# Kernel optimization log

Measured on AMD Instinct MI355X. Metric: run time of the kernel, lower is better.

Reference implementation:

```python
import jax, jax.numpy as jnp
import numpy as np

H = 1024      # hidden_size
V = 50257     # output_size (vocab)
L = 64        # max_length


def setup_inputs() -> dict:
    key = jax.random.key(0)
    ks = jax.random.split(key, 14)
    s = 1.0 / np.sqrt(H)
    return {
        "input": jax.random.randint(ks[0], (1,), 0, V, dtype=jnp.int64),
        "hidden": jax.random.normal(ks[1], (1, 1, H), dtype=jnp.float32),
        "encoder_outputs": jax.random.normal(ks[2], (L, H), dtype=jnp.float32),
        "emb": jax.random.normal(ks[3], (V, H), dtype=jnp.float32),
        "attn_W": jax.random.normal(ks[4], (L, 2 * H), dtype=jnp.float32) * s,
        "attn_b": jax.random.normal(ks[5], (L,), dtype=jnp.float32) * s,
        "comb_W": jax.random.normal(ks[6], (H, 2 * H), dtype=jnp.float32) * s,
        "comb_b": jax.random.normal(ks[7], (H,), dtype=jnp.float32) * s,
        "w_ih": jax.random.normal(ks[8], (3 * H, H), dtype=jnp.float32) * s,
        "w_hh": jax.random.normal(ks[9], (3 * H, H), dtype=jnp.float32) * s,
        "b_ih": jax.random.normal(ks[10], (3 * H,), dtype=jnp.float32) * s,
        "b_hh": jax.random.normal(ks[11], (3 * H,), dtype=jnp.float32) * s,
        "out_W": jax.random.normal(ks[12], (V, H), dtype=jnp.float32) * s,
        "out_b": jax.random.normal(ks[13], (V,), dtype=jnp.float32) * s,
    }


def reference(input, hidden, encoder_outputs, emb, attn_W, attn_b,
              comb_W, comb_b, w_ih, w_hh, b_ih, b_hh, out_W, out_b):
    # embedded: [1, H]  (dropout is identity, p effectively 0 at inference)
    embedded = emb[input[0]][None, :]
    h0 = hidden[0]  # [1, H]

    # additive-style attention over encoder_outputs [L, H]
    attn_logits = jnp.concatenate([embedded, h0], axis=1) @ attn_W.T + attn_b  # [1, L]
    attn_weights = jax.nn.softmax(attn_logits, axis=1)                          # [1, L]
    attn_applied = attn_weights @ encoder_outputs                               # [1, H]

    x = jnp.concatenate([embedded, attn_applied], axis=1) @ comb_W.T + comb_b  # [1, H]
    x = jax.nn.relu(x)

    # single-step GRU cell (PyTorch gate ordering: r, z, n)
    gi = x @ w_ih.T + b_ih    # [1, 3H]
    gh = h0 @ w_hh.T + b_hh   # [1, 3H]
    i_r, i_z, i_n = jnp.split(gi, 3, axis=1)
    h_r, h_z, h_n = jnp.split(gh, 3, axis=1)
    r = jax.nn.sigmoid(i_r + h_r)
    z = jax.nn.sigmoid(i_z + h_z)
    n = jnp.tanh(i_n + r * h_n)
    h_new = (1.0 - z) * n + z * h0  # [1, H]

    out = jax.nn.log_softmax(h_new @ out_W.T + out_b, axis=1)  # [1, V]
    return out, h_new[None, :, :], attn_weights
```

## Files before the change

kernel.cpp:

```cpp
#include <hip/hip_runtime.h>
#include <math.h>

constexpr int H = 1024;
constexpr int V = 50257;
constexpr int L = 64;

constexpr int NBLKD = 512;

constexpr int OFF_ALOG = 0;
constexpr int OFF_GH   = 64;
constexpr int OFF_X    = 64 + 3 * H;
constexpr int OFF_LOG  = OFF_X + H;
constexpr int OFF_PAIR = OFF_LOG + V;

__device__ __forceinline__ float wsum(float v) {
#pragma unroll
    for (int off = 32; off > 0; off >>= 1) v += __shfl_xor(v, off);
    return v;
}
__device__ __forceinline__ float wmax(float v) {
#pragma unroll
    for (int off = 32; off > 0; off >>= 1) v = fmaxf(v, __shfl_xor(v, off));
    return v;
}

__device__ __forceinline__ float dot4(float4 a, float4 b) {
    return a.x * b.x + a.y * b.y + a.z * b.z + a.w * b.w;
}

__device__ __forceinline__ float dotN(const float* __restrict__ w,
                                      const float* __restrict__ v,
                                      int lane, int n4) {
    const float4* w4 = reinterpret_cast<const float4*>(w);
    const float4* v4 = reinterpret_cast<const float4*>(v);
    float acc = 0.f;
    for (int it = 0; it < n4; ++it)
        acc += dot4(w4[lane + it * 64], v4[lane + it * 64]);
    return acc;
}

__device__ __forceinline__ void dot1024x2(const float* __restrict__ wa,
                                          const float* __restrict__ wb,
                                          const float* __restrict__ v,
                                          int lane, float& oa, float& ob) {
    const float4* a4 = reinterpret_cast<const float4*>(wa);
    const float4* b4 = reinterpret_cast<const float4*>(wb);
    const float4* v4 = reinterpret_cast<const float4*>(v);
    float sa = 0.f, sb = 0.f;
#pragma unroll
    for (int it = 0; it < 4; ++it) {
        const float4 x = a4[lane + it * 64];
        const float4 y = b4[lane + it * 64];
        const float4 u = v4[lane + it * 64];
        sa += dot4(x, u);
        sb += dot4(y, u);
    }
    oa = sa; ob = sb;
}

__device__ __forceinline__ void msmerge(float& m, float& s, float m2, float s2) {
    const float M = fmaxf(m, m2);
    s = s * expf(m - M) + s2 * expf(m2 - M);
    m = M;
}

__global__ __launch_bounds__(256) void kA(const long long* __restrict__ idx_p,
                                          const float* __restrict__ hid,
                                          const float* __restrict__ emb,
                                          const float* __restrict__ attn_W,
                                          const float* __restrict__ attn_b,
                                          const float* __restrict__ w_hh,
                                          const float* __restrict__ b_hh,
                                          float* __restrict__ ws) {
    const int tid = threadIdx.x;
    const int lane = tid & 63, wid = tid >> 6;
    if (blockIdx.x < 64) {
        const int l = blockIdx.x;
        const int idx = (int)idx_p[0];
        const float4* w4 = reinterpret_cast<const float4*>(attn_W + (size_t)l * (2 * H));
        const float4* e4 = reinterpret_cast<const float4*>(emb + (size_t)idx * H);
        const float4* h4 = reinterpret_cast<const float4*>(hid);
        float acc = dot4(w4[tid], e4[tid]) + dot4(w4[tid + 256], h4[tid]);
        acc = wsum(acc);
        __shared__ float sred[4];
        if (lane == 0) sred[wid] = acc;
        __syncthreads();
        if (tid == 0)
            ws[OFF_ALOG + l] = sred[0] + sred[1] + sred[2] + sred[3] + attn_b[l];
    } else {
        __shared__ __align__(16) float4 sv[256];
        sv[tid] = reinterpret_cast<const float4*>(hid)[tid];
        __syncthreads();
        const int row = (blockIdx.x - 64) * 4 + wid;
        float acc = wsum(dotN(w_hh + (size_t)row * H,
                              reinterpret_cast<const float*>(sv), lane, 4));
        if (lane == 0) ws[OFF_GH + row] = acc + b_hh[row];
    }
}

__global__ __launch_bounds__(256) void kB(const long long* __restrict__ idx_p,
                                          const float* __restrict__ emb,
                                          const float* __restrict__ enc,
                                          const float* __restrict__ comb_W,
                                          const float* __restrict__ comb_b,
                                          float* __restrict__ ws,
                                          float* __restrict__ out) {
    __shared__ float wls[L];
    __shared__ __align__(16) float4 sx[512];
    const int tid = threadIdx.x;
    if (tid < L) {
        const float lg = ws[OFF_ALOG + tid];
        const float m = wmax(lg);
        const float e = expf(lg - m);
        const float s = wsum(e);
        wls[tid] = e / s;
        if (blockIdx.x == 0) out[V + H + tid] = e / s;
    }
    __syncthreads();
    const int idx = (int)idx_p[0];
    sx[tid] = reinterpret_cast<const float4*>(emb + (size_t)idx * H)[tid];
    {
        const float4* e4 = reinterpret_cast<const float4*>(enc);
        float4 a4 = {0.f, 0.f, 0.f, 0.f};
#pragma unroll 8
        for (int l = 0; l < L; ++l) {
            const float wl = wls[l];
            const float4 v = e4[l * 256 + tid];
            a4.x += wl * v.x; a4.y += wl * v.y;
            a4.z += wl * v.z; a4.w += wl * v.w;
        }
        sx[256 + tid] = a4;
    }
    __syncthreads();
    const int lane = tid & 63, wid = tid >> 6;
    const int row = blockIdx.x * 4 + wid;
    float acc = wsum(dotN(comb_W + (size_t)row * (2 * H),
                          reinterpret_cast<const float*>(sx), lane, 8));
    if (lane == 0) ws[OFF_X + row] = fmaxf(acc + comb_b[row], 0.f);
}

__global__ __launch_bounds__(768) void kC(const float* __restrict__ w_ih,
                                          const float* __restrict__ b_ih,
                                          const float* __restrict__ hid,
                                          float* __restrict__ ws,
                                          float* __restrict__ out) {
    __shared__ __align__(16) float4 sx4[256];
    __shared__ float gi_s[12];
    const int tid = threadIdx.x;
    if (tid < 256) sx4[tid] = reinterpret_cast<const float4*>(ws + OFF_X)[tid];
    __syncthreads();
    const int lane = tid & 63, wid = tid >> 6;
    const int g = wid >> 2, i = wid & 3;
    const int row = g * H + blockIdx.x * 4 + i;
    float acc = wsum(dotN(w_ih + (size_t)row * H,
                          reinterpret_cast<const float*>(sx4), lane, 4));
    if (lane == 0) gi_s[wid] = acc + b_ih[row];
    __syncthreads();
    if (tid < 4) {
        const int t = blockIdx.x * 4 + tid;
        const float ir = gi_s[tid], iz = gi_s[4 + tid], in_ = gi_s[8 + tid];
        const float hr = ws[OFF_GH + t];
        const float hz = ws[OFF_GH + H + t];
        const float hn = ws[OFF_GH + 2 * H + t];
        const float r = 1.f / (1.f + expf(-(ir + hr)));
        const float z = 1.f / (1.f + expf(-(iz + hz)));
        const float n = tanhf(in_ + r * hn);
        out[V + t] = (1.f - z) * n + z * hid[t];
    }
}

__global__ __launch_bounds__(512, 4) void kD(const float* __restrict__ out_W,
                                             const float* __restrict__ out_b,
                                             const float* __restrict__ hnew,
                                             float* __restrict__ ws) {
    __shared__ __align__(16) float shn[H];
    __shared__ float lds_log[104];
    const int tid = threadIdx.x, lane = tid & 63, wid = tid >> 6;
    const int b = blockIdx.x;
    const int row0 = (int)(((long long)b * V) / NBLKD);
    const int row1 = (int)(((long long)(b + 1) * V) / NBLKD);
    const int nrows = row1 - row0;
    for (int i = tid; i < H; i += 512) shn[i] = hnew[i];
    __syncthreads();
    for (int k = 2 * wid; k < nrows; k += 16) {
        const int r0 = row0 + k;
        const int r1v = r0 + 1;
        const bool has2 = (k + 1) < nrows;
        const int r1 = has2 ? r1v : r0;
        float a0, a1;
        dot1024x2(out_W + (size_t)r0 * H, out_W + (size_t)r1 * H, shn, lane, a0, a1);
        a0 = wsum(a0); a1 = wsum(a1);
        if (lane == 0) {
            const float l0 = a0 + out_b[r0];
            lds_log[k] = l0;
            ws[OFF_LOG + r0] = l0;
            if (has2) {
                const float l1 = a1 + out_b[r1];
                lds_log[k + 1] = l1;
                ws[OFF_LOG + r1] = l1;
            }
        }
    }
    __syncthreads();
    if (wid == 0) {
        float v0 = (lane < nrows) ? lds_log[lane] : -INFINITY;
        float v1 = (64 + lane < nrows) ? lds_log[64 + lane] : -INFINITY;
        const float m = wmax(fmaxf(v0, v1));
        float e = 0.f;
        if (lane < nrows)      e += expf(v0 - m);
        if (64 + lane < nrows) e += expf(v1 - m);
        const float s = wsum(e);
        if (lane == 0) {
            ws[OFF_PAIR + 2 * b] = m;
            ws[OFF_PAIR + 2 * b + 1] = s;
        }
    }
}

__global__ __launch_bounds__(256) void kE(const float* __restrict__ ws,
                                          float* __restrict__ out) {
    const int tid = threadIdx.x, lane = tid & 63, wid = tid >> 6;
    float m = -INFINITY, s = 0.f;
    for (int i = tid; i < NBLKD; i += 256) {
        const float mi = ws[OFF_PAIR + 2 * i];
        const float si = ws[OFF_PAIR + 2 * i + 1];
        if (si > 0.f) msmerge(m, s, mi, si);
    }
#pragma unroll
    for (int off = 32; off > 0; off >>= 1) {
        const float mo = __shfl_xor(m, off);
        const float so = __shfl_xor(s, off);
        if (so > 0.f) msmerge(m, s, mo, so);
    }
    __shared__ float sm[4], ss[4], fin[2];
    if (lane == 0) { sm[wid] = m; ss[wid] = s; }
    __syncthreads();
    if (tid == 0) {
        float M = sm[0], S = ss[0];
        for (int i = 1; i < 4; ++i)
            if (ss[i] > 0.f) msmerge(M, S, sm[i], ss[i]);
        fin[0] = M;
        fin[1] = logf(S);
    }
    __syncthreads();
    const int i = blockIdx.x * 256 + tid;
    if (i < V) out[i] = ws[OFF_LOG + i] - fin[0] - fin[1];
}

extern "C" void kernel_launch(void* const* d_in, const int* in_sizes, int n_in,
                              void* d_out, int out_size, void* d_ws, size_t ws_size,
                              hipStream_t stream) {
    const long long* idx  = (const long long*)d_in[0];
    const float* hid    = (const float*)d_in[1];
    const float* enc    = (const float*)d_in[2];
    const float* emb    = (const float*)d_in[3];
    const float* attn_W = (const float*)d_in[4];
    const float* attn_b = (const float*)d_in[5];
    const float* comb_W = (const float*)d_in[6];
    const float* comb_b = (const float*)d_in[7];
    const float* w_ih   = (const float*)d_in[8];
    const float* w_hh   = (const float*)d_in[9];
    const float* b_ih   = (const float*)d_in[10];
    const float* b_hh   = (const float*)d_in[11];
    const float* out_W  = (const float*)d_in[12];
    const float* out_b  = (const float*)d_in[13];
    float* out = (float*)d_out;
    float* ws  = (float*)d_ws;

    kA<<<64 + 768, 256, 0, stream>>>(idx, hid, emb, attn_W, attn_b, w_hh, b_hh, ws);
    kB<<<256, 256, 0, stream>>>(idx, emb, enc, comb_W, comb_b, ws, out);
    kC<<<256, 768, 0, stream>>>(w_ih, b_ih, hid, ws, out);
    kD<<<NBLKD, 512, 0, stream>>>(out_W, out_b, out + V, ws);
    kE<<<(V + 255) / 256, 256, 0, stream>>>(ws, out);
}
```

Measured before the change: 57.42 us.

## Hoist embedding half of comb matvec into kA and keep h_new in registers

The embedding half of the combine matvec (comb_W[:, :H] @ embedded) depends only on the inputs, so it moves into the first kernel as 256 extra blocks and writes a partial sum to the workspace. kB then only does the attention-applied half and adds the partial, which halves its weight traffic on the critical path. Separately, kD now loads h_new straight into per-lane registers instead of staging it in LDS, which removes a __syncthreads and the shared-memory reads. The cost is a larger kA grid and one extra workspace round trip for the partial sums.

```diff
diff --git a/kernel.cpp b/kernel.cpp
--- a/kernel.cpp
+++ b/kernel.cpp
@@ -9,7 +9,8 @@
 
 constexpr int OFF_ALOG = 0;
 constexpr int OFF_GH   = 64;
-constexpr int OFF_X    = 64 + 3 * H;
+constexpr int OFF_CP   = 64 + 3 * H;
+constexpr int OFF_X    = OFF_CP + H;
 constexpr int OFF_LOG  = OFF_X + H;
 constexpr int OFF_PAIR = OFF_LOG + V;
 
@@ -39,25 +40,6 @@
     return acc;
 }
 
-__device__ __forceinline__ void dot1024x2(const float* __restrict__ wa,
-                                          const float* __restrict__ wb,
-                                          const float* __restrict__ v,
-                                          int lane, float& oa, float& ob) {
-    const float4* a4 = reinterpret_cast<const float4*>(wa);
-    const float4* b4 = reinterpret_cast<const float4*>(wb);
-    const float4* v4 = reinterpret_cast<const float4*>(v);
-    float sa = 0.f, sb = 0.f;
-#pragma unroll
-    for (int it = 0; it < 4; ++it) {
-        const float4 x = a4[lane + it * 64];
-        const float4 y = b4[lane + it * 64];
-        const float4 u = v4[lane + it * 64];
-        sa += dot4(x, u);
-        sb += dot4(y, u);
-    }
-    oa = sa; ob = sb;
-}
-
 __device__ __forceinline__ void msmerge(float& m, float& s, float m2, float s2) {
     const float M = fmaxf(m, m2);
     s = s * expf(m - M) + s2 * expf(m2 - M);
@@ -71,11 +53,13 @@
                                           const float* __restrict__ attn_b,
                                           const float* __restrict__ w_hh,
                                           const float* __restrict__ b_hh,
+                                          const float* __restrict__ comb_W,
                                           float* __restrict__ ws) {
     const int tid = threadIdx.x;
     const int lane = tid & 63, wid = tid >> 6;
-    if (blockIdx.x < 64) {
-        const int l = blockIdx.x;
+    const int b = blockIdx.x;
+    if (b < 64) {
+        const int l = b;
         const int idx = (int)idx_p[0];
         const float4* w4 = reinterpret_cast<const float4*>(attn_W + (size_t)l * (2 * H));
         const float4* e4 = reinterpret_cast<const float4*>(emb + (size_t)idx * H);
@@ -87,26 +71,33 @@
         __syncthreads();
         if (tid == 0)
             ws[OFF_ALOG + l] = sred[0] + sred[1] + sred[2] + sred[3] + attn_b[l];
-    } else {
+    } else if (b < 832) {
         __shared__ __align__(16) float4 sv[256];
         sv[tid] = reinterpret_cast<const float4*>(hid)[tid];
         __syncthreads();
-        const int row = (blockIdx.x - 64) * 4 + wid;
+        const int row = (b - 64) * 4 + wid;
         float acc = wsum(dotN(w_hh + (size_t)row * H,
                               reinterpret_cast<const float*>(sv), lane, 4));
         if (lane == 0) ws[OFF_GH + row] = acc + b_hh[row];
-    }
-}
-
-__global__ __launch_bounds__(256) void kB(const long long* __restrict__ idx_p,
-                                          const float* __restrict__ emb,
-                                          const float* __restrict__ enc,
+    } else {
+        __shared__ __align__(16) float4 se[256];
+        const int idx = (int)idx_p[0];
+        se[tid] = reinterpret_cast<const float4*>(emb + (size_t)idx * H)[tid];
+        __syncthreads();
+        const int row = (b - 832) * 4 + wid;
+        float acc = wsum(dotN(comb_W + (size_t)row * (2 * H),
+                              reinterpret_cast<const float*>(se), lane, 4));
+        if (lane == 0) ws[OFF_CP + row] = acc;
+    }
+}
+
+__global__ __launch_bounds__(256) void kB(const float* __restrict__ enc,
                                           const float* __restrict__ comb_W,
                                           const float* __restrict__ comb_b,
                                           float* __restrict__ ws,
                                           float* __restrict__ out) {
     __shared__ float wls[L];
-    __shared__ __align__(16) float4 sx[512];
+    __shared__ __align__(16) float4 sx[256];
     const int tid = threadIdx.x;
     if (tid < L) {
         const float lg = ws[OFF_ALOG + tid];
@@ -117,8 +108,6 @@
         if (blockIdx.x == 0) out[V + H + tid] = e / s;
     }
     __syncthreads();
-    const int idx = (int)idx_p[0];
-    sx[tid] = reinterpret_cast<const float4*>(emb + (size_t)idx * H)[tid];
     {
         const float4* e4 = reinterpret_cast<const float4*>(enc);
         float4 a4 = {0.f, 0.f, 0.f, 0.f};
@@ -129,14 +118,15 @@
             a4.x += wl * v.x; a4.y += wl * v.y;
             a4.z += wl * v.z; a4.w += wl * v.w;
         }
-        sx[256 + tid] = a4;
+        sx[tid] = a4;
     }
     __syncthreads();
     const int lane = tid & 63, wid = tid >> 6;
     const int row = blockIdx.x * 4 + wid;
-    float acc = wsum(dotN(comb_W + (size_t)row * (2 * H),
-                          reinterpret_cast<const float*>(sx), lane, 8));
-    if (lane == 0) ws[OFF_X + row] = fmaxf(acc + comb_b[row], 0.f);
+    float acc = wsum(dotN(comb_W + (size_t)row * (2 * H) + H,
+                          reinterpret_cast<const float*>(sx), lane, 4));
+    if (lane == 0)
+        ws[OFF_X + row] = fmaxf(acc + ws[OFF_CP + row] + comb_b[row], 0.f);
 }
 
 __global__ __launch_bounds__(768) void kC(const float* __restrict__ w_ih,
@@ -173,29 +163,34 @@
                                              const float* __restrict__ out_b,
                                              const float* __restrict__ hnew,
                                              float* __restrict__ ws) {
-    __shared__ __align__(16) float shn[H];
     __shared__ float lds_log[104];
     const int tid = threadIdx.x, lane = tid & 63, wid = tid >> 6;
     const int b = blockIdx.x;
     const int row0 = (int)(((long long)b * V) / NBLKD);
     const int row1 = (int)(((long long)(b + 1) * V) / NBLKD);
     const int nrows = row1 - row0;
-    for (int i = tid; i < H; i += 512) shn[i] = hnew[i];
-    __syncthreads();
+    const float4* v4 = reinterpret_cast<const float4*>(hnew);
+    const float4 hv0 = v4[lane], hv1 = v4[lane + 64];
+    const float4 hv2 = v4[lane + 128], hv3 = v4[lane + 192];
     for (int k = 2 * wid; k < nrows; k += 16) {
         const int r0 = row0 + k;
-        const int r1v = r0 + 1;
         const bool has2 = (k + 1) < nrows;
-        const int r1 = has2 ? r1v : r0;
-        float a0, a1;
-        dot1024x2(out_W + (size_t)r0 * H, out_W + (size_t)r1 * H, shn, lane, a0, a1);
-        a0 = wsum(a0); a1 = wsum(a1);
+        const int r1 = has2 ? r0 + 1 : r0;
+        const float4* a4 = reinterpret_cast<const float4*>(out_W + (size_t)r0 * H);
+        const float4* b4 = reinterpret_cast<const float4*>(out_W + (size_t)r1 * H);
+        const float4 a0 = a4[lane], a1 = a4[lane + 64];
+        const float4 a2 = a4[lane + 128], a3 = a4[lane + 192];
+        const float4 b0 = b4[lane], b1 = b4[lane + 64];
+        const float4 b2 = b4[lane + 128], b3 = b4[lane + 192];
+        float sa = dot4(a0, hv0) + dot4(a1, hv1) + dot4(a2, hv2) + dot4(a3, hv3);
+        float sb = dot4(b0, hv0) + dot4(b1, hv1) + dot4(b2, hv2) + dot4(b3, hv3);
+        sa = wsum(sa); sb = wsum(sb);
         if (lane == 0) {
-            const float l0 = a0 + out_b[r0];
+            const float l0 = sa + out_b[r0];
             lds_log[k] = l0;
             ws[OFF_LOG + r0] = l0;
             if (has2) {
-                const float l1 = a1 + out_b[r1];
+                const float l1 = sb + out_b[r1];
                 lds_log[k + 1] = l1;
                 ws[OFF_LOG + r1] = l1;
             }
@@ -267,8 +262,9 @@
     float* out = (float*)d_out;
     float* ws  = (float*)d_ws;
 
-    kA<<<64 + 768, 256, 0, stream>>>(idx, hid, emb, attn_W, attn_b, w_hh, b_hh, ws);
-    kB<<<256, 256, 0, stream>>>(idx, emb, enc, comb_W, comb_b, ws, out);
+    kA<<<1088, 256, 0, stream>>>(idx, hid, emb, attn_W, attn_b, w_hh, b_hh,
+                                 comb_W, ws);
+    kB<<<256, 256, 0, stream>>>(enc, comb_W, comb_b, ws, out);
     kC<<<256, 768, 0, stream>>>(w_ih, b_ih, hid, ws, out);
     kD<<<NBLKD, 512, 0, stream>>>(out_W, out_b, out + V, ws);
     kE<<<(V + 255) / 256, 256, 0, stream>>>(ws, out);
```

Result: no change. 56.30 us (median of 2 runs) (-1.9%).
